# Kernel tuning notes

Measured on AMD Instinct MI355X. Metric: run time of the kernel, lower is better.

## Reference

```python
import jax, jax.numpy as jnp
import numpy as np


def bilinear_resize(x, out_h, out_w):
    # x: [B, C, H, W]; matches torch F.interpolate(mode='bilinear', align_corners=False)
    B, C, H, W = x.shape
    ry = jnp.clip((jnp.arange(out_h, dtype=jnp.float32) + 0.5) * (H / out_h) - 0.5, 0.0, H - 1)
    rx = jnp.clip((jnp.arange(out_w, dtype=jnp.float32) + 0.5) * (W / out_w) - 0.5, 0.0, W - 1)
    y0 = jnp.floor(ry).astype(jnp.int32); y1 = jnp.minimum(y0 + 1, H - 1)
    x0 = jnp.floor(rx).astype(jnp.int32); x1 = jnp.minimum(x0 + 1, W - 1)
    wy = (ry - y0)[:, None]  # [out_h,1]
    wx = (rx - x0)[None, :]  # [1,out_w]
    r0 = x[:, :, y0, :]; r1 = x[:, :, y1, :]
    v00 = r0[:, :, :, x0]; v01 = r0[:, :, :, x1]
    v10 = r1[:, :, :, x0]; v11 = r1[:, :, :, x1]
    return (v00 * (1 - wx) + v01 * wx) * (1 - wy) + (v10 * (1 - wx) + v11 * wx) * wy


def setup_inputs() -> dict:
    key0 = jax.random.key(0)
    ks = jax.random.split(key0, 16)
    B, N, C, H = 2, 300, 256, 8
    hw_lvl = np.array([[64, 64], [32, 32], [16, 16]], dtype=np.int64)
    L = int((hw_lvl[:, 0] * hw_lvl[:, 1]).sum())  # 5376
    p = lambda k, sh: (0.02 * jax.random.normal(k, sh, dtype=jnp.float32))
    return {
        'query': jax.random.normal(ks[0], (B, N, C), dtype=jnp.float32),
        'key': jax.random.normal(ks[1], (B, L, C), dtype=jnp.float32),
        'value': jax.random.normal(ks[2], (B, L, C), dtype=jnp.float32),
        'key_padding_mask': jnp.zeros((B, L), dtype=bool),
        'hw_lvl': hw_lvl,
        'Wq': p(ks[3], (C, C)), 'Wk': p(ks[4], (C, C)), 'Wv': p(ks[5], (C, C)),
        'Wp': p(ks[6], (C, C)), 'bp': jnp.zeros((C,), jnp.float32),
        'W1': p(ks[7], (H, H)), 'b1': jnp.zeros((H,), jnp.float32),
        'W2': p(ks[8], (H, H)), 'b2': jnp.zeros((H,), jnp.float32),
        'W3': p(ks[9], (H, H)), 'b3': jnp.zeros((H,), jnp.float32),
        'Wm': p(ks[10], (3 * H, 1)), 'bm': jnp.zeros((1,), jnp.float32),
    }


def reference(query, key, value, key_padding_mask, hw_lvl,
              Wq, Wk, Wv, Wp, bp, W1, b1, W2, b2, W3, b3, Wm, bm):
    hw = np.asarray(hw_lvl)
    h1, wd1 = int(hw[0, 0]), int(hw[0, 1])
    h2, wd2 = int(hw[1, 0]), int(hw[1, 1])
    h3, wd3 = int(hw[2, 0]), int(hw[2, 1])
    w1 = h1 * wd1
    w2 = w1 + h2 * wd2
    B, N, C = query.shape
    L = key.shape[1]
    H = W1.shape[0]
    scale = (C // H) ** -0.5

    q = (query @ Wq).reshape(B, N, H, C // H)
    k = (key @ Wk).reshape(B, L, H, C // H)
    v = (value @ Wv).reshape(B, L, H, C // H)
    attn = jnp.einsum('bnhd,blhd->bhnl', q, k) * scale  # [B,H,N,L]

    ap = attn.transpose(0, 2, 3, 1)  # [B,N,L,H]
    f1 = jax.nn.relu(ap[:, :, :w1] @ W1 + b1)                      # [B,N,w1,H]
    f2 = jax.nn.relu(ap[:, :, w1:w2] @ W2 + b2)                    # [B,N,h2*wd2,H]
    f3 = jax.nn.relu(ap[:, :, w2:] @ W3 + b3)                      # [B,N,h3*wd3,H]
    f2 = f2.transpose(0, 1, 3, 2).reshape(B * N, H, h2, wd2)
    f3 = f3.transpose(0, 1, 3, 2).reshape(B * N, H, h3, wd3)
    f2 = bilinear_resize(f2, h1, wd1).transpose(0, 2, 3, 1).reshape(B, N, w1, H)
    f3 = bilinear_resize(f3, h1, wd1).transpose(0, 2, 3, 1).reshape(B, N, w1, H)
    new_feats = jnp.concatenate([f1, f2, f3], axis=-1)             # [B,N,w1,3H]
    mask = jax.nn.relu(new_feats @ Wm + bm)                        # [B,N,w1,1]

    aw = jax.nn.softmax(attn, axis=-1)                             # [B,H,N,L]
    x = jnp.einsum('bhnl,blhd->bnhd', aw, v).reshape(B, N, C)
    x = x @ Wp + bp
    return x, mask
```

## Files before the change

kernel.cpp:

```cpp
#include <hip/hip_runtime.h>
#include <hip/hip_bf16.h>

typedef __hip_bfloat16 bf16;
typedef __attribute__((ext_vector_type(8))) short short8v;
typedef __attribute__((ext_vector_type(8))) unsigned short ushort8v;
typedef __attribute__((ext_vector_type(4))) unsigned short ushort4v;
typedef __attribute__((ext_vector_type(4))) float float4v;

__device__ __forceinline__ float bfu2f(unsigned short u) {
    union { unsigned int i; float f; } v; v.i = ((unsigned int)u) << 16; return v.f;
}
__device__ __forceinline__ unsigned short f2bfu_rn(float x) {
    union { float f; unsigned int i; } u; u.f = x;
    unsigned int r = (u.i + 0x7FFFu + ((u.i >> 16) & 1u)) >> 16;
    return (unsigned short)r;
}

__global__ __launch_bounds__(256) void cast_wt(
    const float* __restrict__ Wq, const float* __restrict__ Wk,
    const float* __restrict__ Wv, const float* __restrict__ Wp,
    unsigned short* __restrict__ wt)
{
    __shared__ unsigned short tile[64][72];
    const float* W = (blockIdx.z == 0) ? Wq : (blockIdx.z == 1) ? Wk
                   : (blockIdx.z == 2) ? Wv : Wp;
    unsigned short* WT = wt + (size_t)blockIdx.z * 65536;
    const int t = threadIdx.x;
    const int k0 = blockIdx.x * 64, n0 = blockIdx.y * 64;
    {
        const int r = t >> 2, cseg = (t & 3) * 16;
        const float* src = W + (size_t)(k0 + r) * 256 + n0 + cseg;
        #pragma unroll
        for (int j = 0; j < 16; ++j) tile[r][cseg + j] = f2bfu_rn(src[j]);
    }
    __syncthreads();
    {
        const int ch = t & 63, lq = t >> 6;
        ushort8v o0, o1;
        #pragma unroll
        for (int i = 0; i < 8; ++i) o0[i] = tile[lq * 16 + i][ch];
        #pragma unroll
        for (int i = 0; i < 8; ++i) o1[i] = tile[lq * 16 + 8 + i][ch];
        unsigned short* dst = WT + (size_t)(n0 + ch) * 256 + k0 + lq * 16;
        *(ushort8v*)(dst)     = o0;
        *(ushort8v*)(dst + 8) = o1;
    }
}

__device__ __forceinline__ void proj_core(
    const float* __restrict__ aptr, const unsigned short* __restrict__ Wt,
    int nc0, int m16, int quad, float4v acc[8])
{
    #pragma unroll
    for (int i = 0; i < 8; ++i) acc[i] = (float4v){0.f, 0.f, 0.f, 0.f};
    #pragma unroll
    for (int ks = 0; ks < 8; ++ks) {
        float4 a0 = *(const float4*)(aptr + ks * 32);
        float4 a1 = *(const float4*)(aptr + ks * 32 + 4);
        short8v af;
        af[0] = (short)f2bfu_rn(a0.x); af[1] = (short)f2bfu_rn(a0.y);
        af[2] = (short)f2bfu_rn(a0.z); af[3] = (short)f2bfu_rn(a0.w);
        af[4] = (short)f2bfu_rn(a1.x); af[5] = (short)f2bfu_rn(a1.y);
        af[6] = (short)f2bfu_rn(a1.z); af[7] = (short)f2bfu_rn(a1.w);
        #pragma unroll
        for (int i = 0; i < 8; ++i) {
            short8v bfr = *(const short8v*)(Wt + (size_t)(nc0 + i * 16 + m16) * 256 + ks * 32 + quad * 8);
            acc[i] = __builtin_amdgcn_mfma_f32_16x16x32_bf16(af, bfr, acc[i], 0, 0, 0);
        }
    }
}

__global__ __launch_bounds__(256) void proj_all(
    const float* __restrict__ q, const float* __restrict__ k, const float* __restrict__ v,
    const unsigned short* __restrict__ wt,
    unsigned short* __restrict__ qb, unsigned short* __restrict__ kb,
    unsigned short* __restrict__ vt)
{
    const int t = threadIdx.x;
    const int wave = t >> 6, lane = t & 63;
    const int m16 = lane & 15, quad = lane >> 4;
    const int msub = (wave & 1) * 16;
    const int nc0 = (wave >> 1) * 128;
    const int bx = blockIdx.x;

    float4v acc[8];
    if (bx < 19) {
        const int m0 = bx * 32;
        const int arow = min(m0 + msub + m16, 599);
        proj_core(q + (size_t)arow * 256 + quad * 8, wt, nc0, m16, quad, acc);
        #pragma unroll
        for (int i = 0; i < 8; ++i)
            #pragma unroll
            for (int r = 0; r < 4; ++r) {
                int m = m0 + msub + quad * 4 + r;
                if (m < 600)
                    qb[(size_t)m * 256 + nc0 + i * 16 + m16] = f2bfu_rn(acc[i][r]);
            }
    } else if (bx < 355) {
        const int m0 = (bx - 19) * 32;
        proj_core(k + (size_t)(m0 + msub + m16) * 256 + quad * 8, wt + 65536, nc0, m16, quad, acc);
        #pragma unroll
        for (int i = 0; i < 8; ++i)
            #pragma unroll
            for (int r = 0; r < 4; ++r) {
                int m = m0 + msub + quad * 4 + r;
                kb[(size_t)m * 256 + nc0 + i * 16 + m16] = f2bfu_rn(acc[i][r]);
            }
    } else {
        const int m0 = (bx - 355) * 32;
        proj_core(v + (size_t)(m0 + msub + m16) * 256 + quad * 8, wt + 131072, nc0, m16, quad, acc);
        const int bb = (m0 >= 5376) ? 1 : 0;
        const int lcol = m0 - bb * 5376 + msub + quad * 4;
        #pragma unroll
        for (int i = 0; i < 8; ++i) {
            const int ch = nc0 + i * 16 + m16;
            ushort4v p;
            #pragma unroll
            for (int r = 0; r < 4; ++r) p[r] = f2bfu_rn(acc[i][r]);
            *(ushort4v*)(vt + (size_t)(bb * 256 + ch) * 5376 + lcol) = p;
        }
    }
}

__global__ __launch_bounds__(512) void attn_fused(
    const unsigned short* __restrict__ qb, const unsigned short* __restrict__ kb,
    const unsigned short* __restrict__ vt,
    unsigned short* __restrict__ attn, float* __restrict__ xbp, float* __restrict__ Sp)
{
    __shared__ unsigned short probs[8][16 * 236];
    __shared__ float partial[8][64][9];
    __shared__ float SrowP[8][16];

    const int t = threadIdx.x;
    const int wave = t >> 6, lane = t & 63;
    const int n0 = blockIdx.x * 16;
    const int bh = blockIdx.y;
    const int zz = blockIdx.z;
    const int b = bh >> 3, h = bh & 7;
    const int m16 = lane & 15, quad = lane >> 4;
    const float scale = 0.17677669529663687f;

    const unsigned short* qp = qb + (size_t)(b * 300 + min(n0 + m16, 299)) * 256 + h * 32 + quad * 8;
    const short8v qfrag = *(const short8v*)qp;

    const unsigned short* kbase = kb + (size_t)(b * 5376) * 256 + h * 32 + quad * 8;
    const unsigned short* vt0 = vt + (size_t)(b * 256 + h * 32 + m16) * 5376;
    const unsigned short* vt1 = vt0 + (size_t)16 * 5376;

    unsigned short* pw = &probs[wave][0];
    const int lc = zz * 1792 + wave * 224;

    float4v c0 = {0.f, 0.f, 0.f, 0.f};
    float4v c1 = {0.f, 0.f, 0.f, 0.f};
    float sm = 0.f;

    #pragma unroll
    for (int i = 0; i < 14; ++i) {
        const int lcol = lc + i * 16 + m16;
        short8v kf = *(const short8v*)(kbase + (size_t)lcol * 256);
        float4v c = {0.f, 0.f, 0.f, 0.f};
        c = __builtin_amdgcn_mfma_f32_16x16x32_bf16(kf, qfrag, c, 0, 0, 0);
        ushort4v pk;
        #pragma unroll
        for (int r = 0; r < 4; ++r) pk[r] = f2bfu_rn(c[r] * scale);
        *(ushort4v*)(pw + m16 * 236 + i * 16 + quad * 4) = pk;
    }

    {
        const int row = lane >> 2;
        const int n = n0 + row;
        if (n < 300) {
            unsigned short* gdst = attn + ((size_t)(b * 300 + n) * 8 + h) * 5376 + lc;
            const unsigned short* lsrc = pw + row * 236;
            #pragma unroll
            for (int it = 0; it < 7; ++it) {
                const int colk = (lane & 3) * 8 + it * 32;
                *(ushort8v*)(gdst + colk) = *(const ushort8v*)(lsrc + colk);
            }
        }
    }

    #pragma unroll
    for (int step = 0; step < 7; ++step) {
        const int lloc = step * 32 + quad * 8;
        ushort8v ua = *(const ushort8v*)(pw + m16 * 236 + lloc);
        short8v af;
        #pragma unroll
        for (int j = 0; j < 8; ++j) {
            float e = __expf(bfu2f(ua[j]));
            sm += e;
            af[j] = (short)f2bfu_rn(e);
        }
        const int lg = lc + lloc;
        short8v b0 = *(const short8v*)(vt0 + lg);
        short8v b1 = *(const short8v*)(vt1 + lg);
        c0 = __builtin_amdgcn_mfma_f32_16x16x32_bf16(af, b0, c0, 0, 0, 0);
        c1 = __builtin_amdgcn_mfma_f32_16x16x32_bf16(af, b1, c1, 0, 0, 0);
    }

    sm += __shfl_xor(sm, 16);
    sm += __shfl_xor(sm, 32);
    if (lane < 16) SrowP[wave][lane] = sm;
    #pragma unroll
    for (int j = 0; j < 4; ++j) {
        partial[wave][lane][j]     = c0[j];
        partial[wave][lane][4 + j] = c1[j];
    }
    __syncthreads();

    if (t < 64) {
        float acc[8] = {0.f, 0.f, 0.f, 0.f, 0.f, 0.f, 0.f, 0.f};
        #pragma unroll
        for (int w = 0; w < 8; ++w)
            #pragma unroll
            for (int j = 0; j < 8; ++j) acc[j] += partial[w][t][j];

        const int d = t & 15, q = t >> 4;
        float* xplane = xbp + (size_t)zz * 153600;
        float* splane = Sp + (size_t)zz * 4800;
        #pragma unroll
        for (int r = 0; r < 4; ++r) {
            const int row = q * 4 + r;
            const int nn = n0 + row;
            if (nn < 300) {
                float S = 0.f;
                #pragma unroll
                for (int w = 0; w < 8; ++w) S += SrowP[w][row];
                if (d == 0) splane[(size_t)(b * 300 + nn) * 8 + h] = S;
                float* o = xplane + (size_t)(b * 300 + nn) * 256 + h * 32 + d;
                o[0]  = acc[r];
                o[16] = acc[4 + r];
            }
        }
    }
}

__global__ __launch_bounds__(256) void proj_out(
    const float* __restrict__ xbp, const float* __restrict__ Sp,
    const unsigned short* __restrict__ Wtp,
    const float* __restrict__ bp, float* __restrict__ out)
{
    const int t = threadIdx.x;
    const int wave = t >> 6, lane = t & 63;
    const int m16 = lane & 15, quad = lane >> 4;
    const int msub = (wave & 1) * 16;
    const int nc0 = (wave >> 1) * 128;
    const int m0 = blockIdx.x * 32;

    const int arow = min(m0 + msub + m16, 599);
    const float* a0p = xbp + (size_t)arow * 256 + quad * 8;

    float4v acc[8];
    #pragma unroll
    for (int i = 0; i < 8; ++i) acc[i] = (float4v){0.f, 0.f, 0.f, 0.f};

    #pragma unroll
    for (int ks = 0; ks < 8; ++ks) {
        const float S = Sp[(size_t)arow * 8 + ks]
                      + Sp[4800 + (size_t)arow * 8 + ks]
                      + Sp[9600 + (size_t)arow * 8 + ks];
        const float rS = 1.0f / S;
        float a[8];
        #pragma unroll
        for (int half = 0; half < 2; ++half) {
            const float* p = a0p + ks * 32 + half * 4;
            float4 x0 = *(const float4*)(p);
            float4 x1 = *(const float4*)(p + 153600);
            float4 x2 = *(const float4*)(p + 307200);
            a[half * 4 + 0] = (x0.x + x1.x + x2.x) * rS;
            a[half * 4 + 1] = (x0.y + x1.y + x2.y) * rS;
            a[half * 4 + 2] = (x0.z + x1.z + x2.z) * rS;
            a[half * 4 + 3] = (x0.w + x1.w + x2.w) * rS;
        }
        short8v af;
        #pragma unroll
        for (int j = 0; j < 8; ++j) af[j] = (short)f2bfu_rn(a[j]);
        #pragma unroll
        for (int i = 0; i < 8; ++i) {
            short8v bfr = *(const short8v*)(Wtp + (size_t)(nc0 + i * 16 + m16) * 256 + ks * 32 + quad * 8);
            acc[i] = __builtin_amdgcn_mfma_f32_16x16x32_bf16(af, bfr, acc[i], 0, 0, 0);
        }
    }

    #pragma unroll
    for (int i = 0; i < 8; ++i) {
        const float bv = bp[nc0 + i * 16 + m16];
        #pragma unroll
        for (int r = 0; r < 4; ++r) {
            int m = m0 + msub + quad * 4 + r;
            if (m < 600)
                out[(size_t)m * 256 + nc0 + i * 16 + m16] = acc[i][r] + bv;
        }
    }
}

__global__ __launch_bounds__(256) void mask_kernel(
    const bf16* __restrict__ attn,
    const float* __restrict__ W1, const float* __restrict__ b1,
    const float* __restrict__ W2, const float* __restrict__ b2,
    const float* __restrict__ W3, const float* __restrict__ b3,
    const float* __restrict__ Wm, const float* __restrict__ bmp,
    float* __restrict__ out)
{
    __shared__ float g2s[1024];
    __shared__ float g3s[256];
    __shared__ float w1s[64], w2s[64], w3s[64];
    __shared__ float b1s[8], b2s[8], b3s[8];
    __shared__ float wms[24];
    __shared__ float bms;

    const int t  = threadIdx.x;
    const int bn = blockIdx.x;
    const int ph = blockIdx.y;
    const unsigned short* ap = (const unsigned short*)attn + (size_t)bn * 8 * 5376;

    if (t < 64) { w1s[t] = W1[t]; w2s[t] = W2[t]; w3s[t] = W3[t]; }
    if (t < 8)  { b1s[t] = b1[t]; b2s[t] = b2[t]; b3s[t] = b3[t]; }
    if (t < 24) wms[t] = Wm[t];
    if (t == 0) bms = bmp[0];
    __syncthreads();

    {
        const int l2 = t * 4;
        ushort4v u[8];
        #pragma unroll
        for (int hh = 0; hh < 8; ++hh)
            u[hh] = *(const ushort4v*)(ap + hh * 5376 + 4096 + l2);
        #pragma unroll
        for (int pp = 0; pp < 4; ++pp) {
            float g = 0.f;
            #pragma unroll
            for (int hh = 0; hh < 8; ++hh) {
                float s = b2s[hh];
                #pragma unroll
                for (int hp = 0; hp < 8; ++hp) s += bfu2f(u[hp][pp]) * w2s[hp * 8 + hh];
                g += fmaxf(s, 0.f) * wms[8 + hh];
            }
            g2s[l2 + pp] = g;
        }
    }
    if (t < 64) {
        const int l3 = t * 4;
        ushort4v u[8];
        #pragma unroll
        for (int hh = 0; hh < 8; ++hh)
            u[hh] = *(const ushort4v*)(ap + hh * 5376 + 5120 + l3);
        #pragma unroll
        for (int pp = 0; pp < 4; ++pp) {
            float g = 0.f;
            #pragma unroll
            for (int hh = 0; hh < 8; ++hh) {
                float s = b3s[hh];
                #pragma unroll
                for (int hp = 0; hp < 8; ++hp) s += bfu2f(u[hp][pp]) * w3s[hp * 8 + hh];
                g += fmaxf(s, 0.f) * wms[16 + hh];
            }
            g3s[l3 + pp] = g;
        }
    }
    __syncthreads();

    {
        const int p0 = ph * 2048 + t * 8;
        ushort8v u[8];
        #pragma unroll
        for (int hh = 0; hh < 8; ++hh)
            u[hh] = *(const ushort8v*)(ap + hh * 5376 + p0);

        float res[8];
        #pragma unroll
        for (int pp = 0; pp < 8; ++pp) {
            const int p = p0 + pp;
            const int Y = p >> 6, X = p & 63;

            float acc = bms;
            #pragma unroll
            for (int hh = 0; hh < 8; ++hh) {
                float s = b1s[hh];
                #pragma unroll
                for (int hp = 0; hp < 8; ++hp) s += bfu2f(u[hp][pp]) * w1s[hp * 8 + hh];
                acc += fmaxf(s, 0.f) * wms[hh];
            }
            {
                float ry = fminf(fmaxf(0.5f * Y - 0.25f, 0.f), 31.f);
                float rx = fminf(fmaxf(0.5f * X - 0.25f, 0.f), 31.f);
                int y0 = (int)ry, x0 = (int)rx;
                int y1 = min(y0 + 1, 31), x1 = min(x0 + 1, 31);
                float wy = ry - (float)y0, wx = rx - (float)x0;
                acc += (g2s[y0 * 32 + x0] * (1.f - wx) + g2s[y0 * 32 + x1] * wx) * (1.f - wy)
                     + (g2s[y1 * 32 + x0] * (1.f - wx) + g2s[y1 * 32 + x1] * wx) * wy;
            }
            {
                float ry = fminf(fmaxf(0.25f * Y - 0.375f, 0.f), 15.f);
                float rx = fminf(fmaxf(0.25f * X - 0.375f, 0.f), 15.f);
                int y0 = (int)ry, x0 = (int)rx;
                int y1 = min(y0 + 1, 15), x1 = min(x0 + 1, 15);
                float wy = ry - (float)y0, wx = rx - (float)x0;
                acc += (g3s[y0 * 16 + x0] * (1.f - wx) + g3s[y0 * 16 + x1] * wx) * (1.f - wy)
                     + (g3s[y1 * 16 + x0] * (1.f - wx) + g3s[y1 * 16 + x1] * wx) * wy;
            }
            res[pp] = fmaxf(acc, 0.f);
        }
        float* o = out + 153600 + (size_t)bn * 4096 + p0;
        #pragma unroll
        for (int pp = 0; pp < 8; ++pp) o[pp] = res[pp];
    }
}

extern "C" void kernel_launch(void* const* d_in, const int* in_sizes, int n_in,
                              void* d_out, int out_size, void* d_ws, size_t ws_size,
                              hipStream_t stream) {
    const float* query = (const float*)d_in[0];
    const float* key   = (const float*)d_in[1];
    const float* value = (const float*)d_in[2];
    const float* Wq = (const float*)d_in[5];
    const float* Wk = (const float*)d_in[6];
    const float* Wv = (const float*)d_in[7];
    const float* Wp = (const float*)d_in[8];
    const float* bp = (const float*)d_in[9];
    const float* W1 = (const float*)d_in[10];
    const float* b1 = (const float*)d_in[11];
    const float* W2 = (const float*)d_in[12];
    const float* b2 = (const float*)d_in[13];
    const float* W3 = (const float*)d_in[14];
    const float* b3 = (const float*)d_in[15];
    const float* Wm = (const float*)d_in[16];
    const float* bm = (const float*)d_in[17];
    float* out = (float*)d_out;

    char* ws = (char*)d_ws;
    unsigned short* wt = (unsigned short*)(ws);
    bf16*  qb   = (bf16*) (ws + 524288);
    bf16*  kb   = (bf16*) (ws + 831488);
    bf16*  vt   = (bf16*) (ws + 6336512);
    bf16*  attn = (bf16*) (ws + 11841536);
    float* xbp  = (float*)(ws + 63451136);
    float* Sp   = (float*)(ws + 65294336);

    cast_wt<<<dim3(4, 4, 4), 256, 0, stream>>>(Wq, Wk, Wv, Wp, wt);

    proj_all<<<691, 256, 0, stream>>>(query, key, value, wt,
        (unsigned short*)qb, (unsigned short*)kb, (unsigned short*)vt);

    attn_fused<<<dim3(19, 16, 3), 512, 0, stream>>>(
        (const unsigned short*)qb, (const unsigned short*)kb, (const unsigned short*)vt,
        (unsigned short*)attn, xbp, Sp);

    mask_kernel<<<dim3(600, 2), 256, 0, stream>>>(attn, W1, b1, W2, b2, W3, b3, Wm, bm, out);

    proj_out<<<19, 256, 0, stream>>>(xbp, Sp, (const unsigned short*)wt + 196608, bp, out);
}
```

Measured before the change: 210.5 us.

## Split attention L-dimension into 7 chunks with XCD-aware block remapping

The attention kernel now splits the key length into 7 chunks of 768 instead of 3 of 1792, giving 2128 blocks in a flat grid. Block indices are remapped so that each group of 8 consecutive blocks, which are spread round-robin across the chiplets, keeps a given batch-head on the same chiplet, improving L2 reuse of K/V. The output projection now reduces 7 partial sums instead of 3, which adds partial-buffer traffic, and the Sp workspace offset moves to fit the larger buffer.

```diff
diff --git a/kernel.cpp b/kernel.cpp
--- a/kernel.cpp
+++ b/kernel.cpp
@@ -127,15 +127,22 @@
     const unsigned short* __restrict__ vt,
     unsigned short* __restrict__ attn, float* __restrict__ xbp, float* __restrict__ Sp)
 {
-    __shared__ unsigned short probs[8][16 * 236];
+    __shared__ unsigned short probs[8][16 * 104];
     __shared__ float partial[8][64][9];
     __shared__ float SrowP[8][16];
 
     const int t = threadIdx.x;
     const int wave = t >> 6, lane = t & 63;
-    const int n0 = blockIdx.x * 16;
-    const int bh = blockIdx.y;
-    const int zz = blockIdx.z;
+
+    const int i0 = blockIdx.x;
+    const int c = i0 & 7;
+    int m = i0 >> 3;
+    const int half = (m >= 133) ? 1 : 0;
+    const int bh = c * 2 + half;
+    m -= half * 133;
+    const int n0 = (m % 19) * 16;
+    const int zz = m / 19;
+
     const int b = bh >> 3, h = bh & 7;
     const int m16 = lane & 15, quad = lane >> 4;
     const float scale = 0.17677669529663687f;
@@ -148,14 +155,14 @@
     const unsigned short* vt1 = vt0 + (size_t)16 * 5376;
 
     unsigned short* pw = &probs[wave][0];
-    const int lc = zz * 1792 + wave * 224;
+    const int lc = zz * 768 + wave * 96;
 
     float4v c0 = {0.f, 0.f, 0.f, 0.f};
     float4v c1 = {0.f, 0.f, 0.f, 0.f};
     float sm = 0.f;
 
     #pragma unroll
-    for (int i = 0; i < 14; ++i) {
+    for (int i = 0; i < 6; ++i) {
         const int lcol = lc + i * 16 + m16;
         short8v kf = *(const short8v*)(kbase + (size_t)lcol * 256);
         float4v c = {0.f, 0.f, 0.f, 0.f};
@@ -163,7 +170,7 @@
         ushort4v pk;
         #pragma unroll
         for (int r = 0; r < 4; ++r) pk[r] = f2bfu_rn(c[r] * scale);
-        *(ushort4v*)(pw + m16 * 236 + i * 16 + quad * 4) = pk;
+        *(ushort4v*)(pw + m16 * 104 + i * 16 + quad * 4) = pk;
     }
 
     {
@@ -171,9 +178,9 @@
         const int n = n0 + row;
         if (n < 300) {
             unsigned short* gdst = attn + ((size_t)(b * 300 + n) * 8 + h) * 5376 + lc;
-            const unsigned short* lsrc = pw + row * 236;
-            #pragma unroll
-            for (int it = 0; it < 7; ++it) {
+            const unsigned short* lsrc = pw + row * 104;
+            #pragma unroll
+            for (int it = 0; it < 3; ++it) {
                 const int colk = (lane & 3) * 8 + it * 32;
                 *(ushort8v*)(gdst + colk) = *(const ushort8v*)(lsrc + colk);
             }
@@ -181,9 +188,9 @@
     }
 
     #pragma unroll
-    for (int step = 0; step < 7; ++step) {
+    for (int step = 0; step < 3; ++step) {
         const int lloc = step * 32 + quad * 8;
-        ushort8v ua = *(const ushort8v*)(pw + m16 * 236 + lloc);
+        ushort8v ua = *(const ushort8v*)(pw + m16 * 104 + lloc);
         short8v af;
         #pragma unroll
         for (int j = 0; j < 8; ++j) {
@@ -256,21 +263,24 @@
 
     #pragma unroll
     for (int ks = 0; ks < 8; ++ks) {
-        const float S = Sp[(size_t)arow * 8 + ks]
-                      + Sp[4800 + (size_t)arow * 8 + ks]
-                      + Sp[9600 + (size_t)arow * 8 + ks];
+        float S = 0.f;
+        #pragma unroll
+        for (int z = 0; z < 7; ++z) S += Sp[(size_t)z * 4800 + (size_t)arow * 8 + ks];
         const float rS = 1.0f / S;
         float a[8];
         #pragma unroll
         for (int half = 0; half < 2; ++half) {
             const float* p = a0p + ks * 32 + half * 4;
-            float4 x0 = *(const float4*)(p);
-            float4 x1 = *(const float4*)(p + 153600);
-            float4 x2 = *(const float4*)(p + 307200);
-            a[half * 4 + 0] = (x0.x + x1.x + x2.x) * rS;
-            a[half * 4 + 1] = (x0.y + x1.y + x2.y) * rS;
-            a[half * 4 + 2] = (x0.z + x1.z + x2.z) * rS;
-            a[half * 4 + 3] = (x0.w + x1.w + x2.w) * rS;
+            float sx = 0.f, sy = 0.f, sz = 0.f, sw = 0.f;
+            #pragma unroll
+            for (int z = 0; z < 7; ++z) {
+                float4 x = *(const float4*)(p + (size_t)z * 153600);
+                sx += x.x; sy += x.y; sz += x.z; sw += x.w;
+            }
+            a[half * 4 + 0] = sx * rS;
+            a[half * 4 + 1] = sy * rS;
+            a[half * 4 + 2] = sz * rS;
+            a[half * 4 + 3] = sw * rS;
         }
         short8v af;
         #pragma unroll
@@ -435,14 +445,14 @@
     bf16*  vt   = (bf16*) (ws + 6336512);
     bf16*  attn = (bf16*) (ws + 11841536);
     float* xbp  = (float*)(ws + 63451136);
-    float* Sp   = (float*)(ws + 65294336);
+    float* Sp   = (float*)(ws + 67751936);
 
     cast_wt<<<dim3(4, 4, 4), 256, 0, stream>>>(Wq, Wk, Wv, Wp, wt);
 
     proj_all<<<691, 256, 0, stream>>>(query, key, value, wt,
         (unsigned short*)qb, (unsigned short*)kb, (unsigned short*)vt);
 
-    attn_fused<<<dim3(19, 16, 3), 512, 0, stream>>>(
+    attn_fused<<<2128, 512, 0, stream>>>(
         (const unsigned short*)qb, (const unsigned short*)kb, (const unsigned short*)vt,
         (unsigned short*)attn, xbp, Sp);
 
```

Result: slower. 216.3 us (+2.7%).
